# Optimization experiments

Hardware: AMD Instinct MI355X
Metric: run time of the kernel (lower is better)

## Reference

```python
import jax, jax.numpy as jnp
import numpy as np

D = 1024        # node_dim
L = 4           # n_layers
H = 16          # n_heads
HID = 512       # mlp_hidden
NT = 65536      # N_tiles (256x256 board)
U = 4096        # eligible units
NY = 256        # board width


def setup_inputs() -> dict:
    key = jax.random.key(0)
    ks = jax.random.split(key, 32)
    p = lambda i, shape: jax.random.normal(ks[i], shape, jnp.float32) * 0.02
    inp = {
        "node_emb": jax.random.normal(ks[0], (NT, D), jnp.float32),
        "tile_ids": jax.random.randint(ks[1], (U,), 0, NT),
        "entropies": jax.random.uniform(ks[2], (U,), jnp.float32),
        "Ny": NY,
        # input_proj: Linear(D+1, D), torch weight layout (out, in)
        "in_w": p(3, (D, D + 1)), "in_b": p(4, (D,)),
        # per-layer MHA params stacked over L
        "attn_in_w": p(5, (L, 3 * D, D)), "attn_in_b": p(6, (L, 3 * D)),
        "attn_out_w": p(7, (L, D, D)), "attn_out_b": p(8, (L, D)),
        # per-layer FFN: Linear(D, 2D) -> ReLU -> Linear(2D, D)
        "ff_w1": p(9, (L, 2 * D, D)), "ff_b1": p(10, (L, 2 * D)),
        "ff_w2": p(11, (L, D, 2 * D)), "ff_b2": p(12, (L, D)),
        "ln1_g": jnp.ones((L, D), jnp.float32), "ln1_b": jnp.zeros((L, D), jnp.float32),
        "ln2_g": jnp.ones((L, D), jnp.float32), "ln2_b": jnp.zeros((L, D), jnp.float32),
        # score head: D -> HID -> HID -> 1 (mlp_depth=2)
        "sh_w0": p(13, (HID, D)), "sh_b0": p(14, (HID,)),
        "sh_w1": p(15, (HID, HID)), "sh_b1": p(16, (HID,)),
        "sh_w2": p(17, (1, HID)), "sh_b2": p(18, (1,)),
    }
    return inp


def _rope_1d(x, pos):
    half = x.shape[-1] // 2
    theta = 1.0 / (10000.0 ** (jnp.arange(half, dtype=jnp.float32) / half))
    ang = pos[:, None] * theta[None, :]            # (U, half)
    c, s = jnp.cos(ang), jnp.sin(ang)
    x1, x2 = x[..., :half], x[..., half:]
    return jnp.concatenate([x1 * c - x2 * s, x1 * s + x2 * c], axis=-1)


def _ln(x, g, b, eps=1e-5):
    m = x.mean(-1, keepdims=True)
    v = ((x - m) ** 2).mean(-1, keepdims=True)
    return (x - m) / jnp.sqrt(v + eps) * g + b


def reference(node_emb, tile_ids, entropies, Ny, in_w, in_b,
              attn_in_w, attn_in_b, attn_out_w, attn_out_b,
              ff_w1, ff_b1, ff_w2, ff_b2, ln1_g, ln1_b, ln2_g, ln2_b,
              sh_w0, sh_b0, sh_w1, sh_b1, sh_w2, sh_b2):
    u = node_emb[tile_ids]                                   # (U, D)
    x = jnp.concatenate([u, entropies[:, None]], axis=-1) @ in_w.T + in_b
    n_units, d = x.shape
    half = d // 2
    hd = d // H
    rows = (tile_ids // Ny).astype(jnp.float32)
    cols = (tile_ids % Ny).astype(jnp.float32)
    for l in range(L):
        # 2D RoPE: row rotation on first half of dims, col rotation on second
        xr = jnp.concatenate([_rope_1d(x[:, :half], rows),
                              _rope_1d(x[:, half:], cols)], axis=-1)
        wq, wk, wv = jnp.split(attn_in_w[l], 3, axis=0)
        bq, bk, bv = jnp.split(attn_in_b[l], 3, axis=0)
        q = (xr @ wq.T + bq).reshape(n_units, H, hd)
        k = (xr @ wk.T + bk).reshape(n_units, H, hd)
        v = (x @ wv.T + bv).reshape(n_units, H, hd)          # V from un-roped x
        scores = jnp.einsum("qhd,khd->hqk", q, k) / jnp.sqrt(jnp.float32(hd))
        attn = jax.nn.softmax(scores, axis=-1)
        o = jnp.einsum("hqk,khd->qhd", attn, v).reshape(n_units, d)
        o = o @ attn_out_w[l].T + attn_out_b[l]
        x = _ln(x + o, ln1_g[l], ln1_b[l])
        h = jax.nn.relu(x @ ff_w1[l].T + ff_b1[l]) @ ff_w2[l].T + ff_b2[l]
        x = _ln(x + h, ln2_g[l], ln2_b[l])
    h = jax.nn.relu(x @ sh_w0.T + sh_b0)
    h = jax.nn.relu(h @ sh_w1.T + sh_b1)
    logits = (h @ sh_w2.T + sh_b2).squeeze(-1)               # (U,)
    probs = jax.nn.softmax(logits)
    entropy = -(probs * jnp.log(probs + 1e-12)).sum()
    return (probs, entropy, logits)
```

## Files before the change

### kernel.cpp

```cpp
#include <hip/hip_runtime.h>
#include <hip/hip_bf16.h>
#include <math.h>

#define UN 4096
#define DN 1024
#define LN_ 4
#define HN 16
#define HD 64

typedef __attribute__((ext_vector_type(8))) short bf16x8;
typedef __attribute__((ext_vector_type(4))) float f32x4;

#define LGKM0 asm volatile("s_waitcnt lgkmcnt(0)" ::: "memory")
#define BARRIER0 __builtin_amdgcn_s_barrier()
#define SCHED0 __builtin_amdgcn_sched_barrier(0)

__device__ __forceinline__ short f2bf(float f) {
  union { float f; unsigned u; } x; x.f = f;
  unsigned r = x.u + 0x7fffu + ((x.u >> 16) & 1u);
  return (short)(r >> 16);
}
__device__ __forceinline__ float bf2f(short b) {
  union { unsigned u; float f; } x; x.u = ((unsigned)(unsigned short)b) << 16;
  return x.f;
}

__device__ __forceinline__ void gload16(const void* g, void* l) {
  __builtin_amdgcn_global_load_lds(
      (const __attribute__((address_space(1))) void*)g,
      (__attribute__((address_space(3))) void*)l, 16, 0, 0);
}

__global__ __launch_bounds__(256)
void convw_kernel(const float* __restrict__ src, short* __restrict__ dst)
{
  int i = blockIdx.x * 256 + threadIdx.x;
  float4 f0 = ((const float4*)src)[i * 2];
  float4 f1 = ((const float4*)src)[i * 2 + 1];
  bf16x8 o;
  o[0] = f2bf(f0.x); o[1] = f2bf(f0.y); o[2] = f2bf(f0.z); o[3] = f2bf(f0.w);
  o[4] = f2bf(f1.x); o[5] = f2bf(f1.y); o[6] = f2bf(f1.z); o[7] = f2bf(f1.w);
  ((bf16x8*)dst)[i] = o;
}

__global__ __launch_bounds__(256)
void convw_in_kernel(const float* __restrict__ src, short* __restrict__ dst)
{
  int idx = blockIdx.x * 256 + threadIdx.x;
  int r = idx >> 10, c = idx & 1023;
  dst[idx] = f2bf(src[r * 1025 + c]);
}

template<int TM>
__global__ __launch_bounds__(256)
void gemm_bf16(const short* __restrict__ A, int lda,
               const short* __restrict__ W, int ldw,
               const float* __restrict__ bias,
               float* __restrict__ C32, short* __restrict__ C16, int ldc,
               int K, int relu,
               const float* __restrict__ ent, const float* __restrict__ wcol,
               int wstride)
{
  constexpr int MBF = TM / 32;
  constexpr int AIN = TM / 64;
  constexpr int NLD = AIN + 2;
  __shared__ __align__(16) short As[2][TM][32];
  __shared__ __align__(16) short Ws[2][128][32];

  const int tid  = threadIdx.x;
  const int bm = blockIdx.x, bn = blockIdx.y;
  const int lane = tid & 63, wave = tid >> 6;
  const int n = lane & 15, quad = lane >> 4;
  const int mw = (wave >> 1) * (TM / 2), nw = (wave & 1) * 64;

  f32x4 acc[MBF][4];
#pragma unroll
  for (int mb = 0; mb < MBF; mb++)
#pragma unroll
    for (int nb = 0; nb < 4; nb++)
#pragma unroll
      for (int r = 0; r < 4; r++) acc[mb][nb][r] = 0.f;

  const int sr = lane >> 2;
  const int sc = (lane & 3) * 8;
  const short* aSrc[AIN];
#pragma unroll
  for (int i = 0; i < AIN; i++)
    aSrc[i] = A + (size_t)(bm * TM + wave * (16 * AIN) + i * 16 + sr) * lda + sc;
  const short* wSrc[2];
#pragma unroll
  for (int i = 0; i < 2; i++)
    wSrc[i] = W + (size_t)(bn * 128 + wave * 32 + i * 16 + sr) * ldw + sc;

  auto stage = [&](int buf, int kk) {
#pragma unroll
    for (int i = 0; i < AIN; i++)
      gload16(aSrc[i] + kk, &As[buf][wave * (16 * AIN) + i * 16][0]);
#pragma unroll
    for (int i = 0; i < 2; i++)
      gload16(wSrc[i] + kk, &Ws[buf][wave * 32 + i * 16][0]);
  };

  stage(0, 0);
  int cur = 0;
  for (int kk = 0; kk < K; kk += 32) {
    if (kk + 32 < K) {
      stage(cur ^ 1, kk + 32);
      asm volatile("s_waitcnt vmcnt(%0)" :: "n"(NLD) : "memory");
    } else {
      asm volatile("s_waitcnt vmcnt(0)" ::: "memory");
    }
    BARRIER0; SCHED0;

    bf16x8 af[MBF], bfr[4];
#pragma unroll
    for (int mb = 0; mb < MBF; mb++) af[mb] = *(bf16x8*)&As[cur][mw + mb * 16 + n][quad * 8];
#pragma unroll
    for (int nb = 0; nb < 4; nb++)   bfr[nb] = *(bf16x8*)&Ws[cur][nw + nb * 16 + n][quad * 8];
#pragma unroll
    for (int mb = 0; mb < MBF; mb++)
#pragma unroll
      for (int nb = 0; nb < 4; nb++)
        acc[mb][nb] = __builtin_amdgcn_mfma_f32_16x16x32_bf16(af[mb], bfr[nb], acc[mb][nb], 0, 0, 0);

    LGKM0; BARRIER0; SCHED0;
    cur ^= 1;
  }

#pragma unroll
  for (int mb = 0; mb < MBF; mb++) {
    float entv[4];
#pragma unroll
    for (int r = 0; r < 4; r++)
      entv[r] = ent ? ent[bm * TM + mw + mb * 16 + quad * 4 + r] : 0.f;
#pragma unroll
    for (int nb = 0; nb < 4; nb++) {
      const int col = bn * 128 + nw + nb * 16 + n;
      const float bs = bias[col];
      const float wc = ent ? wcol[(size_t)col * wstride] : 0.f;
#pragma unroll
      for (int r = 0; r < 4; r++) {
        const int row = bm * TM + mw + mb * 16 + quad * 4 + r;
        float v = acc[mb][nb][r] + bs;
        if (ent)  v += entv[r] * wc;
        if (relu) v = fmaxf(v, 0.f);
        if (C32) C32[(size_t)row * ldc + col] = v;
        if (C16) C16[(size_t)row * ldc + col] = f2bf(v);
      }
    }
  }
}

__global__ __launch_bounds__(256)
void gather_conv_kernel(const float* __restrict__ emb, const int* __restrict__ ids,
                        short* __restrict__ dst)
{
  int idx = blockIdx.x * 256 + threadIdx.x;
  int u = idx >> 10;
  dst[idx] = f2bf(emb[(size_t)ids[u] * 1024 + (idx & 1023)]);
}

__global__ __launch_bounds__(256)
void rope_kernel(const float* __restrict__ x, short* __restrict__ xr,
                 const int* __restrict__ ids, const int* __restrict__ nyp)
{
  int idx = blockIdx.x * 256 + threadIdx.x;
  int u = idx >> 10, j = idx & 1023;
  int blk = j >> 9, o = j & 511;
  int i = o & 255;
  int t = ids[u];
  int ny = *nyp;
  float pos = (blk == 0) ? (float)(t / ny) : (float)(t % ny);
  float theta = expf((float)i * -0.0359778921f);
  float ang = pos * theta;
  float c = cosf(ang), sn = sinf(ang);
  const float* xrow = x + (size_t)u * 1024 + blk * 512;
  float x1 = xrow[i];
  float x2 = xrow[256 + i];
  xr[idx] = f2bf((o < 256) ? (x1 * c - x2 * sn) : (x1 * sn + x2 * c));
}

__global__ __launch_bounds__(256)
void attn_mfma_kernel(const short* __restrict__ qk, const short* __restrict__ v,
                      short* __restrict__ o)
{
  __shared__ __align__(16) short Kt[64][64];
  __shared__ __align__(16) short Vt[64][64];
  __shared__ __align__(16) short Pb[4][16][64];

  const int tid  = threadIdx.x;
  const int lane = tid & 63;
  const int wave = tid >> 6;

  int wg = blockIdx.x + 64 * blockIdx.y;
  wg = (wg & 7) * 128 + (wg >> 3);
  const int qb   = wg & 63;
  const int head = wg >> 6;

  const int n    = lane & 15;
  const int quad = lane >> 4;

  bf16x8 qfrag[2];
  {
    const int qrow = qb * 64 + wave * 16 + n;
    const short* qptr = qk + (size_t)qrow * 2048 + head * 64 + quad * 8;
#pragma unroll
    for (int c = 0; c < 2; c++)
#pragma unroll
      for (int j = 0; j < 8; j++)
        qfrag[c][j] = f2bf(bf2f(qptr[c * 32 + j]) * 0.125f);
  }

  float m_r[4], l_r[4];
  f32x4 o_acc[4];
#pragma unroll
  for (int r = 0; r < 4; r++) { m_r[r] = -3.0e38f; l_r[r] = 0.f; }
#pragma unroll
  for (int nb = 0; nb < 4; nb++)
#pragma unroll
    for (int r = 0; r < 4; r++) o_acc[nb][r] = 0.f;

  const int skey = tid & 63;
  const int sd0  = wave * 16;
  const int krx  = (skey & 7) << 4;

  char* KtB = (char*)&Kt[0][0];
  char* VtB = (char*)&Vt[0][0];
  char* PbB = (char*)&Pb[wave][0][0];

  auto loadT = [&](int kt, bf16x8& k0, bf16x8& k1, bf16x8& v0, bf16x8& v1) {
    const short* kp = qk + (size_t)(kt * 64 + skey) * 2048 + 1024 + head * 64 + sd0;
    k0 = *(const bf16x8*)(kp);
    k1 = *(const bf16x8*)(kp + 8);
    const short* vp = v + (size_t)(kt * 64 + skey) * 1024 + head * 64 + sd0;
    v0 = *(const bf16x8*)(vp);
    v1 = *(const bf16x8*)(vp + 8);
  };

  auto writeT = [&](bf16x8 k0, bf16x8 k1, bf16x8 v0, bf16x8 v1) {
    *(bf16x8*)(KtB + skey * 128 + ((sd0 * 2)      ^ krx)) = k0;
    *(bf16x8*)(KtB + skey * 128 + ((sd0 * 2 + 16) ^ krx)) = k1;
#pragma unroll
    for (int i = 0; i < 8; i++) {
      int d = sd0 + i;
      *(short*)(VtB + d * 128 + ((2 * skey) ^ ((d & 7) << 4))) = v0[i];
    }
#pragma unroll
    for (int i = 0; i < 8; i++) {
      int d = sd0 + 8 + i;
      *(short*)(VtB + d * 128 + ((2 * skey) ^ ((d & 7) << 4))) = v1[i];
    }
  };

  auto computeT = [&]() {
    f32x4 s[4];
#pragma unroll
    for (int nb = 0; nb < 4; nb++) {
      const int row = nb * 16 + n;
      const int rx = (n & 7) << 4;
      bf16x8 k0 = *(bf16x8*)(KtB + row * 128 + ((quad * 16)      ^ rx));
      bf16x8 k1 = *(bf16x8*)(KtB + row * 128 + ((64 + quad * 16) ^ rx));
      f32x4 z = {0.f, 0.f, 0.f, 0.f};
      __builtin_amdgcn_s_setprio(1);
      z = __builtin_amdgcn_mfma_f32_16x16x32_bf16(qfrag[0], k0, z, 0, 0, 0);
      z = __builtin_amdgcn_mfma_f32_16x16x32_bf16(qfrag[1], k1, z, 0, 0, 0);
      __builtin_amdgcn_s_setprio(0);
      s[nb] = z;
    }

    float tl[4];
#pragma unroll
    for (int r = 0; r < 4; r++)
      tl[r] = fmaxf(fmaxf(s[0][r], s[1][r]), fmaxf(s[2][r], s[3][r]));
    bool grow = (tl[0] > m_r[0] + 8.f) || (tl[1] > m_r[1] + 8.f) ||
                (tl[2] > m_r[2] + 8.f) || (tl[3] > m_r[3] + 8.f);
    if (__any(grow)) {
#pragma unroll
      for (int r = 0; r < 4; r++) {
        float t = tl[r];
        t = fmaxf(t, __shfl_xor(t, 1));
        t = fmaxf(t, __shfl_xor(t, 2));
        t = fmaxf(t, __shfl_xor(t, 4));
        t = fmaxf(t, __shfl_xor(t, 8));
        float mnew = fmaxf(m_r[r], t);
        float al = __expf(m_r[r] - mnew);
        m_r[r] = mnew;
        l_r[r] *= al;
#pragma unroll
        for (int nb = 0; nb < 4; nb++) o_acc[nb][r] *= al;
      }
    }

#pragma unroll
    for (int nb = 0; nb < 4; nb++) {
      float p0 = __expf(s[nb][0] - m_r[0]);
      float p1 = __expf(s[nb][1] - m_r[1]);
      float p2 = __expf(s[nb][2] - m_r[2]);
      float p3 = __expf(s[nb][3] - m_r[3]);
      l_r[0] += p0; l_r[1] += p1; l_r[2] += p2; l_r[3] += p3;
      unsigned u01, u23;
      asm("v_cvt_pk_bf16_f32 %0, %1, %2" : "=v"(u01) : "v"(p0), "v"(p1));
      asm("v_cvt_pk_bf16_f32 %0, %1, %2" : "=v"(u23) : "v"(p2), "v"(p3));
      const int colb = 2 * (nb * 16 + n);
      const int r0 = quad * 4;
      *(short*)(PbB + (r0 + 0) * 128 + (colb ^ (((r0 + 0) & 7) << 4))) = (short)(u01 & 0xffff);
      *(short*)(PbB + (r0 + 1) * 128 + (colb ^ (((r0 + 1) & 7) << 4))) = (short)(u01 >> 16);
      *(short*)(PbB + (r0 + 2) * 128 + (colb ^ (((r0 + 2) & 7) << 4))) = (short)(u23 & 0xffff);
      *(short*)(PbB + (r0 + 3) * 128 + (colb ^ (((r0 + 3) & 7) << 4))) = (short)(u23 >> 16);
    }

#pragma unroll
    for (int c = 0; c < 2; c++) {
      const int prx = (n & 7) << 4;
      bf16x8 pf = *(bf16x8*)(PbB + n * 128 + ((64 * c + 16 * quad) ^ prx));
#pragma unroll
      for (int nb = 0; nb < 4; nb++) {
        const int row = nb * 16 + n;
        const int rx = (n & 7) << 4;
        bf16x8 vf = *(bf16x8*)(VtB + row * 128 + ((64 * c + 16 * quad) ^ rx));
        __builtin_amdgcn_s_setprio(1);
        o_acc[nb] = __builtin_amdgcn_mfma_f32_16x16x32_bf16(pf, vf, o_acc[nb], 0, 0, 0);
        __builtin_amdgcn_s_setprio(0);
      }
    }
  };

  bf16x8 ka0, ka1, va0, va1, kb0, kb1, vb0, vb1;
  loadT(0, ka0, ka1, va0, va1);
  for (int kt = 0; kt < 64; kt += 2) {
    LGKM0; BARRIER0; SCHED0;
    writeT(ka0, ka1, va0, va1);
    loadT(kt + 1, kb0, kb1, vb0, vb1);
    LGKM0; BARRIER0; SCHED0;
    computeT();

    LGKM0; BARRIER0; SCHED0;
    writeT(kb0, kb1, vb0, vb1);
    if (kt + 2 < 64) loadT(kt + 2, ka0, ka1, va0, va1);
    LGKM0; BARRIER0; SCHED0;
    computeT();
  }

#pragma unroll
  for (int r = 0; r < 4; r++) {
    float t = l_r[r];
    t += __shfl_xor(t, 1); t += __shfl_xor(t, 2);
    t += __shfl_xor(t, 4); t += __shfl_xor(t, 8);
    l_r[r] = 1.f / t;
  }
#pragma unroll
  for (int nb = 0; nb < 4; nb++)
#pragma unroll
    for (int r = 0; r < 4; r++) {
      int row = qb * 64 + wave * 16 + quad * 4 + r;
      o[(size_t)row * 1024 + head * 64 + nb * 16 + n] = f2bf(o_acc[nb][r] * l_r[r]);
    }
}

__global__ __launch_bounds__(256)
void add_ln_kernel(float* __restrict__ x, const float* __restrict__ d,
                   const float* __restrict__ g, const float* __restrict__ b,
                   short* __restrict__ xb)
{
  __shared__ float sb[4];
  const int row = blockIdx.x, tid = threadIdx.x;
  float* xr = x + (size_t)row * 1024;
  const float* dr = d + (size_t)row * 1024;

  float v[4]; float s = 0.f, ss = 0.f;
#pragma unroll
  for (int i = 0; i < 4; i++) {
    int c = tid + 256 * i;
    v[i] = xr[c] + dr[c];
    s += v[i]; ss += v[i] * v[i];
  }
#pragma unroll
  for (int off = 32; off; off >>= 1) { s += __shfl_down(s, off); ss += __shfl_down(ss, off); }
  const int lane = tid & 63, wid = tid >> 6;
  if (lane == 0) sb[wid] = s;
  __syncthreads();
  s = sb[0] + sb[1] + sb[2] + sb[3];
  __syncthreads();
  if (lane == 0) sb[wid] = ss;
  __syncthreads();
  ss = sb[0] + sb[1] + sb[2] + sb[3];

  float mean = s * (1.f / 1024.f);
  float var  = ss * (1.f / 1024.f) - mean * mean;
  float inv  = rsqrtf(var + 1e-5f);
#pragma unroll
  for (int i = 0; i < 4; i++) {
    int c = tid + 256 * i;
    float o = (v[i] - mean) * inv * g[c] + b[c];
    xr[c] = o;
    xb[(size_t)row * 1024 + c] = f2bf(o);
  }
}

__global__ __launch_bounds__(256)
void logits_kernel(const float* __restrict__ h1, const float* __restrict__ w2,
                   const float* __restrict__ b2, float* __restrict__ out)
{
  const int lane = threadIdx.x & 63;
  const int row = blockIdx.x * 4 + (threadIdx.x >> 6);
  const float* hr = h1 + (size_t)row * 512;
  float s = 0.f;
#pragma unroll
  for (int i = 0; i < 8; i++) s += hr[lane + 64 * i] * w2[lane + 64 * i];
#pragma unroll
  for (int off = 32; off; off >>= 1) s += __shfl_down(s, off);
  if (lane == 0) {
    out[4097 + row] = s + b2[0];
  }
}

__global__ __launch_bounds__(1024)
void softmax_entropy_kernel(const float* __restrict__ lg, float* __restrict__ out)
{
  __shared__ float sb[16];
  const int tid = threadIdx.x;
  const int lane = tid & 63, wid = tid >> 6;

  float l0[4];
#pragma unroll
  for (int i = 0; i < 4; i++) l0[i] = lg[tid + 1024 * i];

  float mx = fmaxf(fmaxf(l0[0], l0[1]), fmaxf(l0[2], l0[3]));
#pragma unroll
  for (int off = 32; off; off >>= 1) mx = fmaxf(mx, __shfl_down(mx, off));
  if (lane == 0) sb[wid] = mx;
  __syncthreads();
  if (tid == 0) { float m = sb[0]; for (int i = 1; i < 16; i++) m = fmaxf(m, sb[i]); sb[0] = m; }
  __syncthreads();
  mx = sb[0];
  __syncthreads();

  float e[4], s = 0.f;
#pragma unroll
  for (int i = 0; i < 4; i++) { e[i] = expf(l0[i] - mx); s += e[i]; }
#pragma unroll
  for (int off = 32; off; off >>= 1) s += __shfl_down(s, off);
  if (lane == 0) sb[wid] = s;
  __syncthreads();
  if (tid == 0) { float t = 0.f; for (int i = 0; i < 16; i++) t += sb[i]; sb[0] = t; }
  __syncthreads();
  float inv = 1.f / sb[0];
  __syncthreads();

  float h = 0.f;
#pragma unroll
  for (int i = 0; i < 4; i++) {
    float p = e[i] * inv;
    out[tid + 1024 * i] = p;
    h += p * logf(p + 1e-12f);
  }
#pragma unroll
  for (int off = 32; off; off >>= 1) h += __shfl_down(h, off);
  if (lane == 0) sb[wid] = h;
  __syncthreads();
  if (tid == 0) { float t = 0.f; for (int i = 0; i < 16; i++) t += sb[i]; out[4096] = -t; }
}

extern "C" void kernel_launch(void* const* d_in, const int* in_sizes, int n_in,
                              void* d_out, int out_size, void* d_ws, size_t ws_size,
                              hipStream_t stream)
{
  const float* node_emb   = (const float*)d_in[0];
  const int*   tile_ids   = (const int*)d_in[1];
  const float* entropies  = (const float*)d_in[2];
  const int*   Ny_p       = (const int*)d_in[3];
  const float* in_w       = (const float*)d_in[4];
  const float* in_b       = (const float*)d_in[5];
  const float* attn_in_w  = (const float*)d_in[6];
  const float* attn_in_b  = (const float*)d_in[7];
  const float* attn_out_w = (const float*)d_in[8];
  const float* attn_out_b = (const float*)d_in[9];
  const float* ff_w1      = (const float*)d_in[10];
  const float* ff_b1      = (const float*)d_in[11];
  const float* ff_w2      = (const float*)d_in[12];
  const float* ff_b2      = (const float*)d_in[13];
  const float* ln1_g      = (const float*)d_in[14];
  const float* ln1_b      = (const float*)d_in[15];
  const float* ln2_g      = (const float*)d_in[16];
  const float* ln2_b      = (const float*)d_in[17];
  const float* sh_w0      = (const float*)d_in[18];
  const float* sh_b0      = (const float*)d_in[19];
  const float* sh_w1      = (const float*)d_in[20];
  const float* sh_b1      = (const float*)d_in[21];
  const float* sh_w2      = (const float*)d_in[22];
  const float* sh_b2      = (const float*)d_in[23];
  float* out = (float*)d_out;

  char* w8 = (char*)d_ws;
  float* X    = (float*)(w8);
  short* Xb   = (short*)(w8 + (16u << 20));
  short* XRb  = (short*)(w8 + (24u << 20));
  short* QKb  = (short*)(w8 + (32u << 20));
  short* Vb   = (short*)(w8 + (48u << 20));
  short* Ob   = (short*)(w8 + (56u << 20));
  float* O2   = (float*)(w8 + (64u << 20));
  short* Wb   = (short*)(w8 + (80u << 20));
  short* Hb   = QKb;
  short* A0b  = Ob;
  short* H0b  = XRb;
  float* H1   = (float*)(w8 + (32u << 20));

  gather_conv_kernel<<<UN * DN / 256, 256, 0, stream>>>(node_emb, tile_ids, A0b);

  convw_in_kernel<<<DN * DN / 256, 256, 0, stream>>>(in_w, Wb);
  gemm_bf16<64><<<dim3(64, 8), 256, 0, stream>>>(A0b, 1024, Wb, 1024, in_b,
      X, Xb, 1024, 1024, 0, entropies, in_w + 1024, 1025);

  for (int l = 0; l < LN_; l++) {
    const float* b_qkv = attn_in_b + (size_t)l * 3 * DN;

    convw_kernel<<<3 * DN * DN / 2048, 256, 0, stream>>>(attn_in_w + (size_t)l * 3 * DN * DN, Wb);
    rope_kernel<<<UN * DN / 256, 256, 0, stream>>>(X, XRb, tile_ids, Ny_p);
    gemm_bf16<128><<<dim3(32, 16), 256, 0, stream>>>(XRb, 1024, Wb, 1024, b_qkv,
        nullptr, QKb, 2048, 1024, 0, nullptr, nullptr, 0);
    gemm_bf16<64><<<dim3(64, 8), 256, 0, stream>>>(Xb, 1024, Wb + (size_t)2048 * 1024, 1024,
        b_qkv + 2048, nullptr, Vb, 1024, 1024, 0, nullptr, nullptr, 0);
    attn_mfma_kernel<<<dim3(UN / 64, HN), 256, 0, stream>>>(QKb, Vb, Ob);
    convw_kernel<<<DN * DN / 2048, 256, 0, stream>>>(attn_out_w + (size_t)l * DN * DN, Wb);
    gemm_bf16<64><<<dim3(64, 8), 256, 0, stream>>>(Ob, 1024, Wb, 1024,
        attn_out_b + (size_t)l * DN, O2, nullptr, 1024, 1024, 0, nullptr, nullptr, 0);
    add_ln_kernel<<<UN, 256, 0, stream>>>(X, O2, ln1_g + (size_t)l * DN, ln1_b + (size_t)l * DN, Xb);
    convw_kernel<<<2 * DN * DN / 2048, 256, 0, stream>>>(ff_w1 + (size_t)l * 2 * DN * DN, Wb);
    gemm_bf16<128><<<dim3(32, 16), 256, 0, stream>>>(Xb, 1024, Wb, 1024,
        ff_b1 + (size_t)l * 2 * DN, nullptr, Hb, 2048, 1024, 1, nullptr, nullptr, 0);
    convw_kernel<<<2 * DN * DN / 2048, 256, 0, stream>>>(ff_w2 + (size_t)l * DN * 2 * DN, Wb);
    gemm_bf16<64><<<dim3(64, 8), 256, 0, stream>>>(Hb, 2048, Wb, 2048,
        ff_b2 + (size_t)l * DN, O2, nullptr, 1024, 2048, 0, nullptr, nullptr, 0);
    add_ln_kernel<<<UN, 256, 0, stream>>>(X, O2, ln2_g + (size_t)l * DN, ln2_b + (size_t)l * DN, Xb);
  }

  convw_kernel<<<512 * DN / 2048, 256, 0, stream>>>(sh_w0, Wb);
  gemm_bf16<64><<<dim3(64, 4), 256, 0, stream>>>(Xb, 1024, Wb, 1024, sh_b0,
      nullptr, H0b, 512, 1024, 1, nullptr, nullptr, 0);
  convw_kernel<<<512 * 512 / 2048, 256, 0, stream>>>(sh_w1, Wb);
  gemm_bf16<64><<<dim3(64, 4), 256, 0, stream>>>(H0b, 512, Wb, 512, sh_b1,
      H1, nullptr, 512, 512, 1, nullptr, nullptr, 0);
  logits_kernel<<<UN / 4, 256, 0, stream>>>(H1, sh_w2, sh_b2, out);
  softmax_entropy_kernel<<<1, 1024, 0, stream>>>(out + 4097, out);
}
```

Measured before the change: 1.968 ms.

## Produce V transposed from GEMM and process 128 queries per attention block

The V projection GEMM swaps its operands so it writes V already transposed (head-dim major, ldc 4096), with a new per-row bias argument carrying the V bias. The attention kernel can then load K and V tiles with 16-byte vector stores into LDS instead of scattering V element by element. Each wave now handles two 16-query groups, so every K/V tile staged in LDS is reused across 128 queries per block and half as many blocks are launched. This costs more registers per thread and possibly lower occupancy.

```diff
diff --git a/kernel.cpp b/kernel.cpp
--- a/kernel.cpp
+++ b/kernel.cpp
@@ -59,7 +59,7 @@
                float* __restrict__ C32, short* __restrict__ C16, int ldc,
                int K, int relu,
                const float* __restrict__ ent, const float* __restrict__ wcol,
-               int wstride)
+               int wstride, const float* __restrict__ rbias)
 {
   constexpr int MBF = TM / 32;
   constexpr int AIN = TM / 64;
@@ -129,19 +129,22 @@
 
 #pragma unroll
   for (int mb = 0; mb < MBF; mb++) {
-    float entv[4];
-#pragma unroll
-    for (int r = 0; r < 4; r++)
-      entv[r] = ent ? ent[bm * TM + mw + mb * 16 + quad * 4 + r] : 0.f;
+    float entv[4], rbv[4];
+#pragma unroll
+    for (int r = 0; r < 4; r++) {
+      const int row = bm * TM + mw + mb * 16 + quad * 4 + r;
+      entv[r] = ent ? ent[row] : 0.f;
+      rbv[r]  = rbias ? rbias[row] : 0.f;
+    }
 #pragma unroll
     for (int nb = 0; nb < 4; nb++) {
       const int col = bn * 128 + nw + nb * 16 + n;
-      const float bs = bias[col];
+      const float bs = bias ? bias[col] : 0.f;
       const float wc = ent ? wcol[(size_t)col * wstride] : 0.f;
 #pragma unroll
       for (int r = 0; r < 4; r++) {
         const int row = bm * TM + mw + mb * 16 + quad * 4 + r;
-        float v = acc[mb][nb][r] + bs;
+        float v = acc[mb][nb][r] + bs + rbv[r];
         if (ent)  v += entv[r] * wc;
         if (relu) v = fmaxf(v, 0.f);
         if (C32) C32[(size_t)row * ldc + col] = v;
@@ -181,145 +184,152 @@
 }
 
 __global__ __launch_bounds__(256)
-void attn_mfma_kernel(const short* __restrict__ qk, const short* __restrict__ v,
+void attn_mfma_kernel(const short* __restrict__ qk, const short* __restrict__ vt,
                       short* __restrict__ o)
 {
   __shared__ __align__(16) short Kt[64][64];
   __shared__ __align__(16) short Vt[64][64];
-  __shared__ __align__(16) short Pb[4][16][64];
+  __shared__ __align__(16) short Pb[4][32][64];
 
   const int tid  = threadIdx.x;
   const int lane = tid & 63;
   const int wave = tid >> 6;
 
-  int wg = blockIdx.x + 64 * blockIdx.y;
-  wg = (wg & 7) * 128 + (wg >> 3);
-  const int qb   = wg & 63;
-  const int head = wg >> 6;
+  int wg = blockIdx.x + 32 * blockIdx.y;
+  wg = (wg & 7) * 64 + (wg >> 3);
+  const int qb   = wg & 31;
+  const int head = wg >> 5;
 
   const int n    = lane & 15;
   const int quad = lane >> 4;
 
-  bf16x8 qfrag[2];
-  {
-    const int qrow = qb * 64 + wave * 16 + n;
+  const int srow = 16 * wave + (lane >> 3);
+  const int scb  = (lane & 7) * 16;
+  const int sdst = srow * 128 + (scb ^ ((srow & 7) << 4));
+
+  bf16x8 qfrag[2][2];
+#pragma unroll
+  for (int qg = 0; qg < 2; qg++) {
+    const int qrow = qb * 128 + wave * 32 + qg * 16 + n;
     const short* qptr = qk + (size_t)qrow * 2048 + head * 64 + quad * 8;
 #pragma unroll
     for (int c = 0; c < 2; c++)
 #pragma unroll
       for (int j = 0; j < 8; j++)
-        qfrag[c][j] = f2bf(bf2f(qptr[c * 32 + j]) * 0.125f);
-  }
-
-  float m_r[4], l_r[4];
-  f32x4 o_acc[4];
-#pragma unroll
-  for (int r = 0; r < 4; r++) { m_r[r] = -3.0e38f; l_r[r] = 0.f; }
-#pragma unroll
-  for (int nb = 0; nb < 4; nb++)
-#pragma unroll
-    for (int r = 0; r < 4; r++) o_acc[nb][r] = 0.f;
-
-  const int skey = tid & 63;
-  const int sd0  = wave * 16;
-  const int krx  = (skey & 7) << 4;
+        qfrag[qg][c][j] = f2bf(bf2f(qptr[c * 32 + j]) * 0.125f);
+  }
+
+  float m_r[2][4], l_r[2][4];
+  f32x4 o_acc[2][4];
+#pragma unroll
+  for (int qg = 0; qg < 2; qg++)
+#pragma unroll
+    for (int r = 0; r < 4; r++) { m_r[qg][r] = -3.0e38f; l_r[qg][r] = 0.f; }
+#pragma unroll
+  for (int qg = 0; qg < 2; qg++)
+#pragma unroll
+    for (int nb = 0; nb < 4; nb++)
+#pragma unroll
+      for (int r = 0; r < 4; r++) o_acc[qg][nb][r] = 0.f;
 
   char* KtB = (char*)&Kt[0][0];
   char* VtB = (char*)&Vt[0][0];
   char* PbB = (char*)&Pb[wave][0][0];
 
   auto loadT = [&](int kt, bf16x8& k0, bf16x8& k1, bf16x8& v0, bf16x8& v1) {
-    const short* kp = qk + (size_t)(kt * 64 + skey) * 2048 + 1024 + head * 64 + sd0;
+    const char* kp = (const char*)(qk + (size_t)(kt * 64 + srow) * 2048
+                                   + 1024 + head * 64) + scb;
     k0 = *(const bf16x8*)(kp);
-    k1 = *(const bf16x8*)(kp + 8);
-    const short* vp = v + (size_t)(kt * 64 + skey) * 1024 + head * 64 + sd0;
+    k1 = *(const bf16x8*)(kp + 8 * 2048 * 2);
+    const char* vp = (const char*)(vt + (size_t)(head * 64 + srow) * 4096
+                                   + kt * 64) + scb;
     v0 = *(const bf16x8*)(vp);
-    v1 = *(const bf16x8*)(vp + 8);
+    v1 = *(const bf16x8*)(vp + 8 * 4096 * 2);
   };
 
   auto writeT = [&](bf16x8 k0, bf16x8 k1, bf16x8 v0, bf16x8 v1) {
-    *(bf16x8*)(KtB + skey * 128 + ((sd0 * 2)      ^ krx)) = k0;
-    *(bf16x8*)(KtB + skey * 128 + ((sd0 * 2 + 16) ^ krx)) = k1;
-#pragma unroll
-    for (int i = 0; i < 8; i++) {
-      int d = sd0 + i;
-      *(short*)(VtB + d * 128 + ((2 * skey) ^ ((d & 7) << 4))) = v0[i];
-    }
-#pragma unroll
-    for (int i = 0; i < 8; i++) {
-      int d = sd0 + 8 + i;
-      *(short*)(VtB + d * 128 + ((2 * skey) ^ ((d & 7) << 4))) = v1[i];
-    }
+    *(bf16x8*)(KtB + sdst)        = k0;
+    *(bf16x8*)(KtB + sdst + 1024) = k1;
+    *(bf16x8*)(VtB + sdst)        = v0;
+    *(bf16x8*)(VtB + sdst + 1024) = v1;
   };
 
   auto computeT = [&]() {
-    f32x4 s[4];
+    f32x4 s[2][4];
 #pragma unroll
     for (int nb = 0; nb < 4; nb++) {
       const int row = nb * 16 + n;
-      const int rx = (n & 7) << 4;
-      bf16x8 k0 = *(bf16x8*)(KtB + row * 128 + ((quad * 16)      ^ rx));
-      bf16x8 k1 = *(bf16x8*)(KtB + row * 128 + ((64 + quad * 16) ^ rx));
-      f32x4 z = {0.f, 0.f, 0.f, 0.f};
+      const int rx = (row & 7) << 4;
+      bf16x8 k0 = *(bf16x8*)(KtB + row * 128 + ((16 * quad) ^ rx));
+      bf16x8 k1 = *(bf16x8*)(KtB + row * 128 + ((64 + 16 * quad) ^ rx));
       __builtin_amdgcn_s_setprio(1);
-      z = __builtin_amdgcn_mfma_f32_16x16x32_bf16(qfrag[0], k0, z, 0, 0, 0);
-      z = __builtin_amdgcn_mfma_f32_16x16x32_bf16(qfrag[1], k1, z, 0, 0, 0);
+#pragma unroll
+      for (int qg = 0; qg < 2; qg++) {
+        f32x4 z = {0.f, 0.f, 0.f, 0.f};
+        z = __builtin_amdgcn_mfma_f32_16x16x32_bf16(qfrag[qg][0], k0, z, 0, 0, 0);
+        z = __builtin_amdgcn_mfma_f32_16x16x32_bf16(qfrag[qg][1], k1, z, 0, 0, 0);
+        s[qg][nb] = z;
+      }
       __builtin_amdgcn_s_setprio(0);
-      s[nb] = z;
-    }
-
-    float tl[4];
-#pragma unroll
-    for (int r = 0; r < 4; r++)
-      tl[r] = fmaxf(fmaxf(s[0][r], s[1][r]), fmaxf(s[2][r], s[3][r]));
-    bool grow = (tl[0] > m_r[0] + 8.f) || (tl[1] > m_r[1] + 8.f) ||
-                (tl[2] > m_r[2] + 8.f) || (tl[3] > m_r[3] + 8.f);
-    if (__any(grow)) {
-#pragma unroll
-      for (int r = 0; r < 4; r++) {
-        float t = tl[r];
-        t = fmaxf(t, __shfl_xor(t, 1));
-        t = fmaxf(t, __shfl_xor(t, 2));
-        t = fmaxf(t, __shfl_xor(t, 4));
-        t = fmaxf(t, __shfl_xor(t, 8));
-        float mnew = fmaxf(m_r[r], t);
-        float al = __expf(m_r[r] - mnew);
-        m_r[r] = mnew;
-        l_r[r] *= al;
-#pragma unroll
-        for (int nb = 0; nb < 4; nb++) o_acc[nb][r] *= al;
+    }
+
+#pragma unroll
+    for (int qg = 0; qg < 2; qg++) {
+      float tl[4];
+#pragma unroll
+      for (int r = 0; r < 4; r++)
+        tl[r] = fmaxf(fmaxf(s[qg][0][r], s[qg][1][r]), fmaxf(s[qg][2][r], s[qg][3][r]));
+      bool grow = (tl[0] > m_r[qg][0] + 8.f) || (tl[1] > m_r[qg][1] + 8.f) ||
+                  (tl[2] > m_r[qg][2] + 8.f) || (tl[3] > m_r[qg][3] + 8.f);
+      if (__any(grow)) {
+#pragma unroll
+        for (int r = 0; r < 4; r++) {
+          float t = tl[r];
+          t = fmaxf(t, __shfl_xor(t, 1));
+          t = fmaxf(t, __shfl_xor(t, 2));
+          t = fmaxf(t, __shfl_xor(t, 4));
+          t = fmaxf(t, __shfl_xor(t, 8));
+          float mnew = fmaxf(m_r[qg][r], t);
+          float al = __expf(m_r[qg][r] - mnew);
+          m_r[qg][r] = mnew;
+          l_r[qg][r] *= al;
+#pragma unroll
+          for (int nb = 0; nb < 4; nb++) o_acc[qg][nb][r] *= al;
+        }
       }
-    }
-
-#pragma unroll
-    for (int nb = 0; nb < 4; nb++) {
-      float p0 = __expf(s[nb][0] - m_r[0]);
-      float p1 = __expf(s[nb][1] - m_r[1]);
-      float p2 = __expf(s[nb][2] - m_r[2]);
-      float p3 = __expf(s[nb][3] - m_r[3]);
-      l_r[0] += p0; l_r[1] += p1; l_r[2] += p2; l_r[3] += p3;
-      unsigned u01, u23;
-      asm("v_cvt_pk_bf16_f32 %0, %1, %2" : "=v"(u01) : "v"(p0), "v"(p1));
-      asm("v_cvt_pk_bf16_f32 %0, %1, %2" : "=v"(u23) : "v"(p2), "v"(p3));
-      const int colb = 2 * (nb * 16 + n);
-      const int r0 = quad * 4;
-      *(short*)(PbB + (r0 + 0) * 128 + (colb ^ (((r0 + 0) & 7) << 4))) = (short)(u01 & 0xffff);
-      *(short*)(PbB + (r0 + 1) * 128 + (colb ^ (((r0 + 1) & 7) << 4))) = (short)(u01 >> 16);
-      *(short*)(PbB + (r0 + 2) * 128 + (colb ^ (((r0 + 2) & 7) << 4))) = (short)(u23 & 0xffff);
-      *(short*)(PbB + (r0 + 3) * 128 + (colb ^ (((r0 + 3) & 7) << 4))) = (short)(u23 >> 16);
+
+#pragma unroll
+      for (int nb = 0; nb < 4; nb++) {
+        float p0 = __expf(s[qg][nb][0] - m_r[qg][0]);
+        float p1 = __expf(s[qg][nb][1] - m_r[qg][1]);
+        float p2 = __expf(s[qg][nb][2] - m_r[qg][2]);
+        float p3 = __expf(s[qg][nb][3] - m_r[qg][3]);
+        l_r[qg][0] += p0; l_r[qg][1] += p1; l_r[qg][2] += p2; l_r[qg][3] += p3;
+        unsigned u01, u23;
+        asm("v_cvt_pk_bf16_f32 %0, %1, %2" : "=v"(u01) : "v"(p0), "v"(p1));
+        asm("v_cvt_pk_bf16_f32 %0, %1, %2" : "=v"(u23) : "v"(p2), "v"(p3));
+        const int colb = 2 * (nb * 16 + n);
+        const int r0 = qg * 16 + quad * 4;
+        *(short*)(PbB + (r0 + 0) * 128 + (colb ^ (((r0 + 0) & 7) << 4))) = (short)(u01 & 0xffff);
+        *(short*)(PbB + (r0 + 1) * 128 + (colb ^ (((r0 + 1) & 7) << 4))) = (short)(u01 >> 16);
+        *(short*)(PbB + (r0 + 2) * 128 + (colb ^ (((r0 + 2) & 7) << 4))) = (short)(u23 & 0xffff);
+        *(short*)(PbB + (r0 + 3) * 128 + (colb ^ (((r0 + 3) & 7) << 4))) = (short)(u23 >> 16);
+      }
     }
 
 #pragma unroll
     for (int c = 0; c < 2; c++) {
       const int prx = (n & 7) << 4;
-      bf16x8 pf = *(bf16x8*)(PbB + n * 128 + ((64 * c + 16 * quad) ^ prx));
+      bf16x8 pf0 = *(bf16x8*)(PbB + n * 128 + ((64 * c + 16 * quad) ^ prx));
+      bf16x8 pf1 = *(bf16x8*)(PbB + (16 + n) * 128 + ((64 * c + 16 * quad) ^ prx));
 #pragma unroll
       for (int nb = 0; nb < 4; nb++) {
-        const int row = nb * 16 + n;
-        const int rx = (n & 7) << 4;
-        bf16x8 vf = *(bf16x8*)(VtB + row * 128 + ((64 * c + 16 * quad) ^ rx));
+        const int vrow = nb * 16 + n;
+        const int vrx = (vrow & 7) << 4;
+        bf16x8 vf = *(bf16x8*)(VtB + vrow * 128 + ((64 * c + 16 * quad) ^ vrx));
         __builtin_amdgcn_s_setprio(1);
-        o_acc[nb] = __builtin_amdgcn_mfma_f32_16x16x32_bf16(pf, vf, o_acc[nb], 0, 0, 0);
+        o_acc[0][nb] = __builtin_amdgcn_mfma_f32_16x16x32_bf16(pf0, vf, o_acc[0][nb], 0, 0, 0);
+        o_acc[1][nb] = __builtin_amdgcn_mfma_f32_16x16x32_bf16(pf1, vf, o_acc[1][nb], 0, 0, 0);
         __builtin_amdgcn_s_setprio(0);
       }
     }
@@ -342,19 +352,23 @@
   }
 
 #pragma unroll
-  for (int r = 0; r < 4; r++) {
-    float t = l_r[r];
-    t += __shfl_xor(t, 1); t += __shfl_xor(t, 2);
-    t += __shfl_xor(t, 4); t += __shfl_xor(t, 8);
-    l_r[r] = 1.f / t;
-  }
-#pragma unroll
-  for (int nb = 0; nb < 4; nb++)
+  for (int qg = 0; qg < 2; qg++)
 #pragma unroll
     for (int r = 0; r < 4; r++) {
-      int row = qb * 64 + wave * 16 + quad * 4 + r;
-      o[(size_t)row * 1024 + head * 64 + nb * 16 + n] = f2bf(o_acc[nb][r] * l_r[r]);
-    }
+      float t = l_r[qg][r];
+      t += __shfl_xor(t, 1); t += __shfl_xor(t, 2);
+      t += __shfl_xor(t, 4); t += __shfl_xor(t, 8);
+      l_r[qg][r] = 1.f / t;
+    }
+#pragma unroll
+  for (int qg = 0; qg < 2; qg++)
+#pragma unroll
+    for (int nb = 0; nb < 4; nb++)
+#pragma unroll
+      for (int r = 0; r < 4; r++) {
+        int row = qb * 128 + wave * 32 + qg * 16 + quad * 4 + r;
+        o[(size_t)row * 1024 + head * 64 + nb * 16 + n] = f2bf(o_acc[qg][nb][r] * l_r[qg][r]);
+      }
 }
 
 __global__ __launch_bounds__(256)
@@ -509,7 +523,7 @@
 
   convw_in_kernel<<<DN * DN / 256, 256, 0, stream>>>(in_w, Wb);
   gemm_bf16<64><<<dim3(64, 8), 256, 0, stream>>>(A0b, 1024, Wb, 1024, in_b,
-      X, Xb, 1024, 1024, 0, entropies, in_w + 1024, 1025);
+      X, Xb, 1024, 1024, 0, entropies, in_w + 1024, 1025, nullptr);
 
   for (int l = 0; l < LN_; l++) {
     const float* b_qkv = attn_in_b + (size_t)l * 3 * DN;
@@ -517,29 +531,29 @@
     convw_kernel<<<3 * DN * DN / 2048, 256, 0, stream>>>(attn_in_w + (size_t)l * 3 * DN * DN, Wb);
     rope_kernel<<<UN * DN / 256, 256, 0, stream>>>(X, XRb, tile_ids, Ny_p);
     gemm_bf16<128><<<dim3(32, 16), 256, 0, stream>>>(XRb, 1024, Wb, 1024, b_qkv,
-        nullptr, QKb, 2048, 1024, 0, nullptr, nullptr, 0);
-    gemm_bf16<64><<<dim3(64, 8), 256, 0, stream>>>(Xb, 1024, Wb + (size_t)2048 * 1024, 1024,
-        b_qkv + 2048, nullptr, Vb, 1024, 1024, 0, nullptr, nullptr, 0);
-    attn_mfma_kernel<<<dim3(UN / 64, HN), 256, 0, stream>>>(QKb, Vb, Ob);
+        nullptr, QKb, 2048, 1024, 0, nullptr, nullptr, 0, nullptr);
+    gemm_bf16<64><<<dim3(16, 32), 256, 0, stream>>>(Wb + (size_t)2048 * 1024, 1024,
+        Xb, 1024, nullptr, nullptr, Vb, 4096, 1024, 0, nullptr, nullptr, 0, b_qkv + 2048);
+    attn_mfma_kernel<<<dim3(32, HN), 256, 0, stream>>>(QKb, Vb, Ob);
     convw_kernel<<<DN * DN / 2048, 256, 0, stream>>>(attn_out_w + (size_t)l * DN * DN, Wb);
     gemm_bf16<64><<<dim3(64, 8), 256, 0, stream>>>(Ob, 1024, Wb, 1024,
-        attn_out_b + (size_t)l * DN, O2, nullptr, 1024, 1024, 0, nullptr, nullptr, 0);
+        attn_out_b + (size_t)l * DN, O2, nullptr, 1024, 1024, 0, nullptr, nullptr, 0, nullptr);
     add_ln_kernel<<<UN, 256, 0, stream>>>(X, O2, ln1_g + (size_t)l * DN, ln1_b + (size_t)l * DN, Xb);
     convw_kernel<<<2 * DN * DN / 2048, 256, 0, stream>>>(ff_w1 + (size_t)l * 2 * DN * DN, Wb);
     gemm_bf16<128><<<dim3(32, 16), 256, 0, stream>>>(Xb, 1024, Wb, 1024,
-        ff_b1 + (size_t)l * 2 * DN, nullptr, Hb, 2048, 1024, 1, nullptr, nullptr, 0);
+        ff_b1 + (size_t)l * 2 * DN, nullptr, Hb, 2048, 1024, 1, nullptr, nullptr, 0, nullptr);
     convw_kernel<<<2 * DN * DN / 2048, 256, 0, stream>>>(ff_w2 + (size_t)l * DN * 2 * DN, Wb);
     gemm_bf16<64><<<dim3(64, 8), 256, 0, stream>>>(Hb, 2048, Wb, 2048,
-        ff_b2 + (size_t)l * DN, O2, nullptr, 1024, 2048, 0, nullptr, nullptr, 0);
+        ff_b2 + (size_t)l * DN, O2, nullptr, 1024, 2048, 0, nullptr, nullptr, 0, nullptr);
     add_ln_kernel<<<UN, 256, 0, stream>>>(X, O2, ln2_g + (size_t)l * DN, ln2_b + (size_t)l * DN, Xb);
   }
 
   convw_kernel<<<512 * DN / 2048, 256, 0, stream>>>(sh_w0, Wb);
   gemm_bf16<64><<<dim3(64, 4), 256, 0, stream>>>(Xb, 1024, Wb, 1024, sh_b0,
-      nullptr, H0b, 512, 1024, 1, nullptr, nullptr, 0);
+      nullptr, H0b, 512, 1024, 1, nullptr, nullptr, 0, nullptr);
   convw_kernel<<<512 * 512 / 2048, 256, 0, stream>>>(sh_w1, Wb);
   gemm_bf16<64><<<dim3(64, 4), 256, 0, stream>>>(H0b, 512, Wb, 512, sh_b1,
-      H1, nullptr, 512, 512, 1, nullptr, nullptr, 0);
+      H1, nullptr, 512, 512, 1, nullptr, nullptr, 0, nullptr);
   logits_kernel<<<UN / 4, 256, 0, stream>>>(H1, sh_w2, sh_b2, out);
   softmax_entropy_kernel<<<1, 1024, 0, stream>>>(out + 4097, out);
 }
```

New measurement: 1.798 ms. 1.09x faster.
